# Performance work log

Measured on AMD Instinct MI355X. Metric: run time of the kernel, lower is better.

The kernel has to match this reference:

```python
import jax, jax.numpy as jnp
import numpy as np


def _interp_linear(c, out_len):
    """PyTorch F.interpolate(mode='linear', align_corners=False) along last axis.
    c: (d, in_len) -> (d, out_len). Half-pixel coordinate mapping."""
    in_len = c.shape[-1]
    scale = in_len / out_len
    src = (jnp.arange(out_len, dtype=jnp.float32) + 0.5) * scale - 0.5
    src = jnp.clip(src, 0.0, in_len - 1)
    lo = jnp.floor(src).astype(jnp.int32)
    hi = jnp.minimum(lo + 1, in_len - 1)
    w = (src - lo.astype(jnp.float32)).astype(c.dtype)
    return c[..., lo] * (1.0 - w) + c[..., hi] * w


def _causal_spectrum(spec, fft_size):
    """Given the real part of a causal kernel's spectrum (1, F, d) with
    F = fft_size//2+1, recover the full complex spectrum via the Hilbert
    transform (analytic-signal window in time domain)."""
    t = jnp.fft.irfft(spec, n=fft_size, axis=1)  # even real kernel (1, fft_size, d)
    w = jnp.ones((fft_size,), dtype=t.dtype)
    w = w.at[1:fft_size // 2].set(2.0)
    w = w.at[fft_size // 2 + 1:].set(0.0)
    return jnp.fft.rfft(t * w[None, :, None], axis=1)  # (1, F, d) complex


def setup_inputs() -> dict:
    key = jax.random.key(0)
    k1, k2 = jax.random.split(key)
    B, N, D, NUM_FREQS = 8, 8192, 512, 512
    x = jax.random.normal(k1, (B, N, D), dtype=jnp.float32)
    coeffs = jax.random.normal(k2, (D, NUM_FREQS), dtype=jnp.float32)
    dc = jnp.ones((D, 1), dtype=jnp.float32)
    return {"x": x, "coeffs": coeffs, "dc": dc}


def reference(x, coeffs, dc):
    n = x.shape[-2]
    fft_size = int(2 ** int(np.ceil(np.log2(2 * n))))
    # interpolate learned real frequency coefficients up to fft_size//2 bins
    pos = _interp_linear(coeffs, fft_size // 2)          # (d, fft_size//2)
    a = jnp.concatenate([dc, pos], axis=1)               # (d, fft_size//2+1)
    a = jnp.transpose(a)[None]                           # (1, F, d)
    spec = _causal_spectrum(a, fft_size)                 # (1, F, d) complex
    xf = jnp.fft.rfft(x, n=fft_size, axis=-2)            # (B, F, d)
    out = jnp.fft.irfft(xf * spec, n=fft_size, axis=-2)  # (B, fft_size, d)
    return out[..., :n, :]
```

## Files before the change

### kernel.cpp

```cpp
#include <hip/hip_runtime.h>


#define SPEC_LEN 8193
constexpr float PI_F = 3.14159265358979323846f;

__device__ __forceinline__ float2 f2add(float2 a, float2 b) { return make_float2(a.x + b.x, a.y + b.y); }
__device__ __forceinline__ float2 f2sub(float2 a, float2 b) { return make_float2(a.x - b.x, a.y - b.y); }
__device__ __forceinline__ float2 cmul(float2 a, float2 b) {
    return make_float2(a.x * b.x - a.y * b.y, a.x * b.y + a.y * b.x);
}

#define SLOT(k) ((((k) & 3) << 2) | ((k) >> 2))

__device__ __forceinline__ int addr1(int n2, int k1) {
    return (n2 << 4) | ((k1 + n2) & 15);
}
__device__ __forceinline__ int addr2(int r, int m2) {
    return (r << 5) | ((m2 + 2 * r) & 31);
}
__device__ __forceinline__ int addr3(int k) {
    int lo = (k + 2 * (k >> 4) + (k >> 8) + (k >> 12)) & 15;
    return (k & ~15) | lo;
}

template <int SGN>
__device__ __forceinline__ void fft4(float2& a, float2& b, float2& c, float2& d) {
    float2 A0 = f2add(a, c), A1 = f2sub(a, c), A2 = f2add(b, d), A3 = f2sub(b, d);
    float2 T = (SGN < 0) ? make_float2(A3.y, -A3.x) : make_float2(-A3.y, A3.x);
    a = f2add(A0, A2); b = f2add(A1, T); c = f2sub(A0, A2); d = f2sub(A1, T);
}

template <int SGN>
__device__ __forceinline__ void fft16_tail(float2* v) {
    const float C1 = 0.9238795325112867f, S1 = 0.3826834323650898f, R2 = 0.7071067811865476f;
    v[5]  = cmul(v[5],  make_float2(C1, SGN < 0 ? -S1 : S1));
    v[6]  = cmul(v[6],  make_float2(R2, SGN < 0 ? -R2 : R2));
    v[7]  = cmul(v[7],  make_float2(S1, SGN < 0 ? -C1 : C1));
    v[9]  = cmul(v[9],  make_float2(R2, SGN < 0 ? -R2 : R2));
    v[10] = (SGN < 0) ? make_float2(v[10].y, -v[10].x) : make_float2(-v[10].y, v[10].x);
    v[11] = cmul(v[11], make_float2(-R2, SGN < 0 ? -R2 : R2));
    v[13] = cmul(v[13], make_float2(S1, SGN < 0 ? -C1 : C1));
    v[14] = cmul(v[14], make_float2(-R2, SGN < 0 ? -R2 : R2));
    v[15] = cmul(v[15], make_float2(-C1, SGN < 0 ? S1 : -S1));
    fft4<SGN>(v[0], v[1], v[2], v[3]);
    fft4<SGN>(v[4], v[5], v[6], v[7]);
    fft4<SGN>(v[8], v[9], v[10], v[11]);
    fft4<SGN>(v[12], v[13], v[14], v[15]);
}
template <int SGN>
__device__ __forceinline__ void fft16(float2* v) {
    fft4<SGN>(v[0], v[4], v[8], v[12]);
    fft4<SGN>(v[1], v[5], v[9], v[13]);
    fft4<SGN>(v[2], v[6], v[10], v[14]);
    fft4<SGN>(v[3], v[7], v[11], v[15]);
    fft16_tail<SGN>(v);
}
template <int SGN>
__device__ __forceinline__ void fft16_half(float2* v) {
    #pragma unroll
    for (int j = 0; j < 4; ++j) {
        float2 a = v[j], b = v[j + 4];
        float2 T = (SGN < 0) ? make_float2(b.y, -b.x) : make_float2(-b.y, b.x);
        v[j] = f2add(a, b); v[j + 4] = f2add(a, T);
        v[j + 8] = f2sub(a, b); v[j + 12] = f2sub(a, T);
    }
    fft16_tail<SGN>(v);
}

__device__ __forceinline__ void twchain(float2* v, float2 w) {
    float2 acc = w;
    v[SLOT(1)] = cmul(v[SLOT(1)], acc);
    #pragma unroll
    for (int k = 2; k < 16; ++k) { acc = cmul(acc, w); v[SLOT(k)] = cmul(v[SLOT(k)], acc); }
}
__device__ __forceinline__ void twchain_nat(float2* v, float2 w) {
    float2 acc = w;
    v[1] = cmul(v[1], acc);
    #pragma unroll
    for (int k = 2; k < 16; ++k) { acc = cmul(acc, w); v[k] = cmul(v[k], acc); }
}

__device__ __forceinline__ float2 shflx1(float2 v) {
    return make_float2(__shfl_xor(v.x, 1), __shfl_xor(v.y, 1));
}

#define W32_TABLES \
    constexpr float WC[16] = {1.f, 0.98078528f, 0.92387953f, 0.83146961f, 0.70710678f, \
        0.55557023f, 0.38268343f, 0.19509032f, 0.f, -0.19509032f, -0.38268343f, \
        -0.55557023f, -0.70710678f, -0.83146961f, -0.92387953f, -0.98078528f}; \
    constexpr float WS[16] = {0.f, 0.19509032f, 0.38268343f, 0.55557023f, 0.70710678f, \
        0.83146961f, 0.92387953f, 0.98078528f, 1.f, 0.98078528f, 0.92387953f, \
        0.83146961f, 0.70710678f, 0.55557023f, 0.38268343f, 0.19509032f};

__device__ __forceinline__ void fwd_L2_L3(float2* sbuf, int tid) {
    {
        int k1 = tid >> 5, m2 = tid & 31;
        float2 u[16];
        #pragma unroll
        for (int m1 = 0; m1 < 16; ++m1) u[m1] = sbuf[addr1(32 * m1 + m2, k1)];
        __syncthreads();
        fft16<-1>(u);
        float sn, cs; __sincosf(-(PI_F / 256.0f) * (float)m2, &sn, &cs);
        twchain(u, make_float2(cs, sn));
        #pragma unroll
        for (int q1 = 0; q1 < 16; ++q1) sbuf[addr2(k1 * 16 + q1, m2)] = u[SLOT(q1)];
        __syncthreads();
    }
    {
        int k1 = tid >> 5, q1 = (tid >> 1) & 15, half = tid & 1;
        float2 e[16];
        #pragma unroll
        for (int j = 0; j < 16; ++j) e[j] = sbuf[addr2(k1 * 16 + q1, 2 * j + half)];
        __syncthreads();
        fft16<-1>(e);
        W32_TABLES
        #pragma unroll
        for (int q = 0; q < 16; ++q) {
            float2 mine = e[SLOT(q)];
            float2 othr = shflx1(mine);
            float2 Eq = half ? othr : mine;
            float2 Oq = half ? mine : othr;
            float2 WO = cmul(make_float2(WC[q], -WS[q]), Oq);
            float2 X = half ? f2sub(Eq, WO) : f2add(Eq, WO);
            int k = k1 + 16 * q1 + 256 * (q + 16 * half);
            sbuf[addr3(k)] = X;
        }
        __syncthreads();
    }
}

__device__ __forceinline__ void inv_L3_L2(float2* sbuf, int tid) {
    {
        int k1 = tid >> 5, q1 = (tid >> 1) & 15, half = tid & 1;
        float2 t[16];
        #pragma unroll
        for (int q = 0; q < 16; ++q)
            t[q] = sbuf[addr3(k1 + 16 * q1 + 256 * (q + 16 * half))];
        __syncthreads();
        W32_TABLES
        #pragma unroll
        for (int q = 0; q < 16; ++q) {
            float2 othr = shflx1(t[q]);
            if (half) t[q] = cmul(make_float2(WC[q], WS[q]), f2sub(othr, t[q]));
            else      t[q] = f2add(t[q], othr);
        }
        fft16<1>(t);
        #pragma unroll
        for (int j = 0; j < 16; ++j) sbuf[addr2(k1 * 16 + q1, 2 * j + half)] = t[SLOT(j)];
        __syncthreads();
    }
    {
        int k1 = tid >> 5, m2 = tid & 31;
        float2 u[16];
        #pragma unroll
        for (int q1 = 0; q1 < 16; ++q1) u[q1] = sbuf[addr2(k1 * 16 + q1, m2)];
        __syncthreads();
        float sn, cs; __sincosf((PI_F / 256.0f) * (float)m2, &sn, &cs);
        twchain_nat(u, make_float2(cs, sn));
        fft16<1>(u);
        #pragma unroll
        for (int m1 = 0; m1 < 16; ++m1) sbuf[addr1(32 * m1 + m2, k1)] = u[SLOT(m1)];
        __syncthreads();
    }
}

__device__ __forceinline__ void inv_L1(const float2* sbuf, int tid, float2* v) {
    #pragma unroll
    for (int k1 = 0; k1 < 16; ++k1) v[k1] = sbuf[addr1(tid, k1)];
    float sn, cs; __sincosf((PI_F / 4096.0f) * (float)tid, &sn, &cs);
    twchain_nat(v, make_float2(cs, sn));
    fft16<1>(v);
}

__device__ __forceinline__ float aval(const float* C, float dcv, int idx) {
    if (idx == 0) return dcv;
    int j = idx - 1;
    float src = ((float)j + 0.5f) * 0.0625f - 0.5f;
    src = fminf(fmaxf(src, 0.0f), 511.0f);
    int lo = (int)floorf(src);
    int hi = min(lo + 1, 511);
    float w = src - (float)lo;
    return C[lo] * (1.0f - w) + C[hi] * w;
}

__global__ __launch_bounds__(512) void k01(const float* __restrict__ x,
                                           const float* __restrict__ coeffs,
                                           const float* __restrict__ dc,
                                           float2* __restrict__ spec,
                                           float2* __restrict__ zin) {
    __shared__ float2 sbuf[8192];
    int tid = threadIdx.x;
    if (blockIdx.x < 512) {
        int d = blockIdx.x;
        const float* C = coeffs + d * 512;
        float dcv = dc[d];
        #pragma unroll
        for (int tt = 0; tt < 16; ++tt) {
            int k = tid + (tt << 9);
            float ak = aval(C, dcv, k);
            float am = aval(C, dcv, 8192 - k);
            float Ae = 0.5f * (ak + am), Ao = 0.5f * (ak - am);
            float sn, cs; __sincosf((PI_F / 8192.0f) * (float)k, &sn, &cs);
            sbuf[addr3(k)] = make_float2(Ae - Ao * sn, Ao * cs);
        }
        __syncthreads();
        inv_L3_L2(sbuf, tid);
        float2 v[16];
        inv_L1(sbuf, tid, v);
        float2 u[16];
        #pragma unroll
        for (int n1 = 0; n1 < 16; ++n1) {
            float2 z = v[SLOT(n1)];
            int n = (n1 << 9) + tid;
            float te = z.x * (1.0f / 8192.0f);
            float to = z.y * (1.0f / 8192.0f);
            int m0 = 2 * n;
            float he = (m0 == 0) ? te : ((m0 < 8192) ? 2.0f * te : ((m0 == 8192) ? te : 0.0f));
            float ho = (m0 + 1 < 8192) ? 2.0f * to : 0.0f;
            u[n1] = make_float2(he, ho);
        }
        fft16<-1>(u);
        float sn, cs; __sincosf(-(PI_F / 4096.0f) * (float)tid, &sn, &cs);
        twchain(u, make_float2(cs, sn));
        #pragma unroll
        for (int k1 = 0; k1 < 16; ++k1) sbuf[addr1(tid, k1)] = u[SLOT(k1)];
        __syncthreads();
        fwd_L2_L3(sbuf, tid);
        float2* Sd = spec + (size_t)d * SPEC_LEN;
        const float scale = 1.0f / 8192.0f;
        #pragma unroll
        for (int tt = 0; tt < 8; ++tt) {
            int k = tid + (tt << 9);
            if (k == 0) {
                float2 Z0 = sbuf[addr3(0)];
                Sd[0]    = make_float2((Z0.x + Z0.y) * scale, 0.0f);
                Sd[8192] = make_float2((Z0.x - Z0.y) * scale, 0.0f);
                float2 Z4 = sbuf[addr3(4096)];
                Sd[4096] = make_float2(Z4.x * scale, -Z4.y * scale);
            } else {
                int km = 8192 - k;
                float2 Zk = sbuf[addr3(k)], Zm = sbuf[addr3(km)];
                float2 Xe = make_float2((Zk.x + Zm.x) * 0.5f, (Zk.y - Zm.y) * 0.5f);
                float2 dz = make_float2((Zk.x - Zm.x) * 0.5f, (Zk.y + Zm.y) * 0.5f);
                float2 Xo = make_float2(dz.y, -dz.x);
                float sn2, cs2; __sincosf(-(PI_F / 8192.0f) * (float)k, &sn2, &cs2);
                float2 wXo = cmul(make_float2(cs2, sn2), Xo);
                Sd[k]  = make_float2((Xe.x + wXo.x) * scale, (Xe.y + wXo.y) * scale);
                Sd[km] = make_float2((Xe.x - wXo.x) * scale, -(Xe.y - wXo.y) * scale);
            }
        }
    } else {
        int bid = blockIdx.x - 512;
        int nt = bid & 127, dt = (bid >> 7) & 7, bb = bid >> 10;
        float* tile = (float*)sbuf;
        const float4* x4 = (const float4*)(x + ((size_t)bb * 8192 + (size_t)nt * 64) * 512 + dt * 64);
        int lane4 = tid & 15, row = tid >> 4;
        #pragma unroll
        for (int r = 0; r < 2; ++r) {
            int rr = row + 32 * r;
            float4 vv = x4[(size_t)rr * 128 + lane4];
            float* dst = &tile[rr * 65 + lane4 * 4];
            dst[0] = vv.x; dst[1] = vv.y; dst[2] = vv.z; dst[3] = vv.w;
        }
        __syncthreads();
        int tx4 = tid & 15, dl = tid >> 4;
        #pragma unroll
        for (int r = 0; r < 2; ++r) {
            int dloc = dl + 32 * r;
            int d = dt * 64 + dloc;
            int npb = nt * 32 + 2 * tx4;
            float4 w;
            w.x = tile[(4 * tx4 + 0) * 65 + dloc];
            w.y = tile[(4 * tx4 + 1) * 65 + dloc];
            w.z = tile[(4 * tx4 + 2) * 65 + dloc];
            w.w = tile[(4 * tx4 + 3) * 65 + dloc];
            *(float4*)&zin[((size_t)(d * 8 + bb)) * 4096 + npb] = w;
        }
    }
}

__global__ __launch_bounds__(512) void k2_conv(const float2* __restrict__ zin,
                                               const float2* __restrict__ spec,
                                               float2* __restrict__ yout) {
    __shared__ float2 sbuf[8192];
    int wg = blockIdx.x, d = wg >> 3, tid = threadIdx.x;
    const float2* zi = zin + (size_t)wg * 4096;
    float2 v[16];
    #pragma unroll
    for (int n1 = 0; n1 < 8; ++n1) v[n1] = zi[(n1 << 9) + tid];
    fft16_half<-1>(v);
    {
        float sn, cs; __sincosf(-(PI_F / 4096.0f) * (float)tid, &sn, &cs);
        twchain(v, make_float2(cs, sn));
    }
    #pragma unroll
    for (int k1 = 0; k1 < 16; ++k1) sbuf[addr1(tid, k1)] = v[SLOT(k1)];
    __syncthreads();
    fwd_L2_L3(sbuf, tid);
    const float2* S = spec + (size_t)d * SPEC_LEN;
    #pragma unroll
    for (int tt = 0; tt < 8; ++tt) {
        int k = tid + (tt << 9);
        if (k == 0) {
            float2 Z0 = sbuf[addr3(0)];
            float X0 = Z0.x + Z0.y, XM = Z0.x - Z0.y;
            float2 S0 = S[0], SM = S[8192];
            float2 Y0 = make_float2(X0 * S0.x, X0 * S0.y);
            float2 YM = make_float2(XM * SM.x, XM * SM.y);
            float2 Ye = make_float2((Y0.x + YM.x) * 0.5f, (Y0.y - YM.y) * 0.5f);
            float2 Yo = make_float2((Y0.x - YM.x) * 0.5f, (Y0.y + YM.y) * 0.5f);
            sbuf[addr3(0)] = make_float2(Ye.x - Yo.y, Ye.y + Yo.x);
            int p4 = addr3(4096);
            float2 Z4 = sbuf[p4];
            float2 Y4 = cmul(make_float2(Z4.x, -Z4.y), S[4096]);
            sbuf[p4] = make_float2(Y4.x, -Y4.y);
        } else {
            int km = 8192 - k;
            int p1 = addr3(k), p2 = addr3(km);
            float2 Zk = sbuf[p1], Zm = sbuf[p2];
            float2 Xe = make_float2((Zk.x + Zm.x) * 0.5f, (Zk.y - Zm.y) * 0.5f);
            float2 dz = make_float2((Zk.x - Zm.x) * 0.5f, (Zk.y + Zm.y) * 0.5f);
            float2 Xo = make_float2(dz.y, -dz.x);
            float sn, cs; __sincosf(-(PI_F / 8192.0f) * (float)k, &sn, &cs);
            float2 w = make_float2(cs, sn);
            float2 wXo = cmul(w, Xo);
            float2 Xk = f2add(Xe, wXo);
            float2 Xm = make_float2(Xe.x - wXo.x, -(Xe.y - wXo.y));
            float2 Yk = cmul(Xk, S[k]);
            float2 Ym = cmul(Xm, S[km]);
            float2 Ye = make_float2((Yk.x + Ym.x) * 0.5f, (Yk.y - Ym.y) * 0.5f);
            float2 dy = make_float2((Yk.x - Ym.x) * 0.5f, (Yk.y + Ym.y) * 0.5f);
            float2 Yo = cmul(make_float2(cs, -sn), dy);
            sbuf[p1] = make_float2(Ye.x - Yo.y, Ye.y + Yo.x);
            sbuf[p2] = make_float2(Ye.x + Yo.y, Yo.x - Ye.y);
        }
    }
    __syncthreads();
    inv_L3_L2(sbuf, tid);
    inv_L1(sbuf, tid, v);
    float2* yo = yout + (size_t)wg * 4096;
    #pragma unroll
    for (int n1 = 0; n1 < 8; ++n1) yo[(n1 << 9) + tid] = v[SLOT(n1)];
}

__global__ __launch_bounds__(512) void k3_unpack(const float2* __restrict__ yout,
                                                 float* __restrict__ out) {
    __shared__ float2 tile[64 * 33];
    int bid = blockIdx.x;
    int nt = bid & 127, dt = (bid >> 7) & 7, bb = bid >> 10;
    int tid = threadIdx.x;
    const float4* y4 = (const float4*)yout;
    int tx4 = tid & 15, dl = tid >> 4;
    #pragma unroll
    for (int r = 0; r < 2; ++r) {
        int dloc = dl + 32 * r;
        int d = dt * 64 + dloc;
        float4 vv = y4[(size_t)(d * 8 + bb) * 2048 + nt * 16 + tx4];
        tile[dloc * 33 + 2 * tx4]     = make_float2(vv.x, vv.y);
        tile[dloc * 33 + 2 * tx4 + 1] = make_float2(vv.z, vv.w);
    }
    __syncthreads();
    const float* tf = (const float*)tile;
    int lane4 = tid & 15, nl = tid >> 4;
    #pragma unroll
    for (int r = 0; r < 2; ++r) {
        int nloc = nl + 32 * r;
        int npl = nloc >> 1, e = nloc & 1;
        float4 w;
        w.x = tf[((4 * lane4 + 0) * 33 + npl) * 2 + e];
        w.y = tf[((4 * lane4 + 1) * 33 + npl) * 2 + e];
        w.z = tf[((4 * lane4 + 2) * 33 + npl) * 2 + e];
        w.w = tf[((4 * lane4 + 3) * 33 + npl) * 2 + e];
        int n = nt * 64 + nloc;
        *(float4*)&out[((size_t)bb * 8192 + n) * 512 + dt * 64 + lane4 * 4] = w;
    }
}

extern "C" void kernel_launch(void* const* d_in, const int* in_sizes, int n_in,
                              void* d_out, int out_size, void* d_ws, size_t ws_size,
                              hipStream_t stream) {
    const float* x      = (const float*)d_in[0];
    const float* coeffs = (const float*)d_in[1];
    const float* dc     = (const float*)d_in[2];
    float* out = (float*)d_out;

    float2* spec = (float2*)d_ws;
    float2* zbuf = (float2*)((char*)d_ws + (size_t)512 * SPEC_LEN * sizeof(float2));

    k01<<<512 + 8192, 512, 0, stream>>>(x, coeffs, dc, spec, zbuf);
    k2_conv<<<4096, 512, 0, stream>>>(zbuf, spec, zbuf);
    k3_unpack<<<8192, 512, 0, stream>>>(zbuf, out);
}
```

Baseline: 530.3 us.

## Precompute twiddle tables, fold real-FFT post-processing into spectrum coefficients, remap blocks

Replaces per-thread sincos twiddle chains with global twiddle tables built by a new init kernel. The spectrum is stored as precomputed P/Q coefficients so the convolution step fuses the real-FFT split/merge and the spectral multiply into fewer complex ops. k2 block indices are remapped by XCD for locality, code moves to ext_vector types, and occupancy hints are added. The cost is an extra kernel launch and extra global table reads, plus a small accuracy change from using table twiddles instead of chained ones.

```diff
diff --git a/kernel.cpp b/kernel.cpp
--- a/kernel.cpp
+++ b/kernel.cpp
@@ -1,14 +1,21 @@
 #include <hip/hip_runtime.h>
 
 
-#define SPEC_LEN 8193
-constexpr float PI_F = 3.14159265358979323846f;
-
-__device__ __forceinline__ float2 f2add(float2 a, float2 b) { return make_float2(a.x + b.x, a.y + b.y); }
-__device__ __forceinline__ float2 f2sub(float2 a, float2 b) { return make_float2(a.x - b.x, a.y - b.y); }
-__device__ __forceinline__ float2 cmul(float2 a, float2 b) {
-    return make_float2(a.x * b.x - a.y * b.y, a.x * b.y + a.y * b.x);
-}
+typedef float v2f __attribute__((ext_vector_type(2)));
+
+#define PQ_STRIDE 4097
+constexpr double PI_D = 3.14159265358979323846;
+
+__device__ v2f    g_twA[15][512];
+__device__ v2f    g_twB[15][32];
+__device__ v2f    g_w81[4096];
+__device__ v2f    g_h[4096];
+__device__ float4 g_u[4097];
+
+__device__ __forceinline__ v2f mkv2(float x, float y) { v2f r; r.x = x; r.y = y; return r; }
+__device__ __forceinline__ v2f cmul(v2f a, v2f b)  { return mkv2(a.x, a.x) * b + mkv2(-a.y, a.y) * b.yx; }
+__device__ __forceinline__ v2f cmulc(v2f a, v2f b) { return mkv2(a.x, -a.x) * b + mkv2(a.y, a.y) * b.yx; }
+__device__ __forceinline__ v2f cmulcA(v2f a, v2f b){ return mkv2(a.x, a.x) * b + mkv2(a.y, -a.y) * b.yx; }
 
 #define SLOT(k) ((((k) & 3) << 2) | ((k) >> 2))
 
@@ -24,31 +31,31 @@
 }
 
 template <int SGN>
-__device__ __forceinline__ void fft4(float2& a, float2& b, float2& c, float2& d) {
-    float2 A0 = f2add(a, c), A1 = f2sub(a, c), A2 = f2add(b, d), A3 = f2sub(b, d);
-    float2 T = (SGN < 0) ? make_float2(A3.y, -A3.x) : make_float2(-A3.y, A3.x);
-    a = f2add(A0, A2); b = f2add(A1, T); c = f2sub(A0, A2); d = f2sub(A1, T);
+__device__ __forceinline__ void fft4(v2f& a, v2f& b, v2f& c, v2f& d) {
+    v2f A0 = a + c, A1 = a - c, A2 = b + d, A3 = b - d;
+    v2f T = (SGN < 0) ? mkv2(A3.y, -A3.x) : mkv2(-A3.y, A3.x);
+    a = A0 + A2; b = A1 + T; c = A0 - A2; d = A1 - T;
 }
 
 template <int SGN>
-__device__ __forceinline__ void fft16_tail(float2* v) {
+__device__ __forceinline__ void fft16_tail(v2f* v) {
     const float C1 = 0.9238795325112867f, S1 = 0.3826834323650898f, R2 = 0.7071067811865476f;
-    v[5]  = cmul(v[5],  make_float2(C1, SGN < 0 ? -S1 : S1));
-    v[6]  = cmul(v[6],  make_float2(R2, SGN < 0 ? -R2 : R2));
-    v[7]  = cmul(v[7],  make_float2(S1, SGN < 0 ? -C1 : C1));
-    v[9]  = cmul(v[9],  make_float2(R2, SGN < 0 ? -R2 : R2));
-    v[10] = (SGN < 0) ? make_float2(v[10].y, -v[10].x) : make_float2(-v[10].y, v[10].x);
-    v[11] = cmul(v[11], make_float2(-R2, SGN < 0 ? -R2 : R2));
-    v[13] = cmul(v[13], make_float2(S1, SGN < 0 ? -C1 : C1));
-    v[14] = cmul(v[14], make_float2(-R2, SGN < 0 ? -R2 : R2));
-    v[15] = cmul(v[15], make_float2(-C1, SGN < 0 ? S1 : -S1));
+    v[5]  = cmul(v[5],  mkv2(C1, SGN < 0 ? -S1 : S1));
+    v[6]  = cmul(v[6],  mkv2(R2, SGN < 0 ? -R2 : R2));
+    v[7]  = cmul(v[7],  mkv2(S1, SGN < 0 ? -C1 : C1));
+    v[9]  = cmul(v[9],  mkv2(R2, SGN < 0 ? -R2 : R2));
+    v[10] = (SGN < 0) ? mkv2(v[10].y, -v[10].x) : mkv2(-v[10].y, v[10].x);
+    v[11] = cmul(v[11], mkv2(-R2, SGN < 0 ? -R2 : R2));
+    v[13] = cmul(v[13], mkv2(S1, SGN < 0 ? -C1 : C1));
+    v[14] = cmul(v[14], mkv2(-R2, SGN < 0 ? -R2 : R2));
+    v[15] = cmul(v[15], mkv2(-C1, SGN < 0 ? S1 : -S1));
     fft4<SGN>(v[0], v[1], v[2], v[3]);
     fft4<SGN>(v[4], v[5], v[6], v[7]);
     fft4<SGN>(v[8], v[9], v[10], v[11]);
     fft4<SGN>(v[12], v[13], v[14], v[15]);
 }
 template <int SGN>
-__device__ __forceinline__ void fft16(float2* v) {
+__device__ __forceinline__ void fft16(v2f* v) {
     fft4<SGN>(v[0], v[4], v[8], v[12]);
     fft4<SGN>(v[1], v[5], v[9], v[13]);
     fft4<SGN>(v[2], v[6], v[10], v[14]);
@@ -56,32 +63,19 @@
     fft16_tail<SGN>(v);
 }
 template <int SGN>
-__device__ __forceinline__ void fft16_half(float2* v) {
+__device__ __forceinline__ void fft16_half(v2f* v) {
     #pragma unroll
     for (int j = 0; j < 4; ++j) {
-        float2 a = v[j], b = v[j + 4];
-        float2 T = (SGN < 0) ? make_float2(b.y, -b.x) : make_float2(-b.y, b.x);
-        v[j] = f2add(a, b); v[j + 4] = f2add(a, T);
-        v[j + 8] = f2sub(a, b); v[j + 12] = f2sub(a, T);
+        v2f a = v[j], b = v[j + 4];
+        v2f T = (SGN < 0) ? mkv2(b.y, -b.x) : mkv2(-b.y, b.x);
+        v[j] = a + b; v[j + 4] = a + T;
+        v[j + 8] = a - b; v[j + 12] = a - T;
     }
     fft16_tail<SGN>(v);
 }
 
-__device__ __forceinline__ void twchain(float2* v, float2 w) {
-    float2 acc = w;
-    v[SLOT(1)] = cmul(v[SLOT(1)], acc);
-    #pragma unroll
-    for (int k = 2; k < 16; ++k) { acc = cmul(acc, w); v[SLOT(k)] = cmul(v[SLOT(k)], acc); }
-}
-__device__ __forceinline__ void twchain_nat(float2* v, float2 w) {
-    float2 acc = w;
-    v[1] = cmul(v[1], acc);
-    #pragma unroll
-    for (int k = 2; k < 16; ++k) { acc = cmul(acc, w); v[k] = cmul(v[k], acc); }
-}
-
-__device__ __forceinline__ float2 shflx1(float2 v) {
-    return make_float2(__shfl_xor(v.x, 1), __shfl_xor(v.y, 1));
+__device__ __forceinline__ v2f shflx1(v2f v) {
+    return mkv2(__shfl_xor(v.x, 1), __shfl_xor(v.y, 1));
 }
 
 #define W32_TABLES \
@@ -92,23 +86,26 @@
         0.83146961f, 0.92387953f, 0.98078528f, 1.f, 0.98078528f, 0.92387953f, \
         0.83146961f, 0.70710678f, 0.55557023f, 0.38268343f, 0.19509032f};
 
-__device__ __forceinline__ void fwd_L2_L3(float2* sbuf, int tid) {
+__device__ __forceinline__ void fwd_L2_L3(v2f* sbuf, int tid) {
     {
         int k1 = tid >> 5, m2 = tid & 31;
-        float2 u[16];
+        v2f w[15];
+        #pragma unroll
+        for (int j = 0; j < 15; ++j) w[j] = g_twB[j][m2];
+        v2f u[16];
         #pragma unroll
         for (int m1 = 0; m1 < 16; ++m1) u[m1] = sbuf[addr1(32 * m1 + m2, k1)];
         __syncthreads();
         fft16<-1>(u);
-        float sn, cs; __sincosf(-(PI_F / 256.0f) * (float)m2, &sn, &cs);
-        twchain(u, make_float2(cs, sn));
+        #pragma unroll
+        for (int k = 1; k < 16; ++k) u[SLOT(k)] = cmul(u[SLOT(k)], w[k - 1]);
         #pragma unroll
         for (int q1 = 0; q1 < 16; ++q1) sbuf[addr2(k1 * 16 + q1, m2)] = u[SLOT(q1)];
         __syncthreads();
     }
     {
         int k1 = tid >> 5, q1 = (tid >> 1) & 15, half = tid & 1;
-        float2 e[16];
+        v2f e[16];
         #pragma unroll
         for (int j = 0; j < 16; ++j) e[j] = sbuf[addr2(k1 * 16 + q1, 2 * j + half)];
         __syncthreads();
@@ -116,12 +113,12 @@
         W32_TABLES
         #pragma unroll
         for (int q = 0; q < 16; ++q) {
-            float2 mine = e[SLOT(q)];
-            float2 othr = shflx1(mine);
-            float2 Eq = half ? othr : mine;
-            float2 Oq = half ? mine : othr;
-            float2 WO = cmul(make_float2(WC[q], -WS[q]), Oq);
-            float2 X = half ? f2sub(Eq, WO) : f2add(Eq, WO);
+            v2f mine = e[SLOT(q)];
+            v2f othr = shflx1(mine);
+            v2f Eq = half ? othr : mine;
+            v2f Oq = half ? mine : othr;
+            v2f WO = cmul(mkv2(WC[q], -WS[q]), Oq);
+            v2f X = half ? Eq - WO : Eq + WO;
             int k = k1 + 16 * q1 + 256 * (q + 16 * half);
             sbuf[addr3(k)] = X;
         }
@@ -129,10 +126,10 @@
     }
 }
 
-__device__ __forceinline__ void inv_L3_L2(float2* sbuf, int tid) {
+__device__ __forceinline__ void inv_L3_L2(v2f* sbuf, int tid) {
     {
         int k1 = tid >> 5, q1 = (tid >> 1) & 15, half = tid & 1;
-        float2 t[16];
+        v2f t[16];
         #pragma unroll
         for (int q = 0; q < 16; ++q)
             t[q] = sbuf[addr3(k1 + 16 * q1 + 256 * (q + 16 * half))];
@@ -140,9 +137,9 @@
         W32_TABLES
         #pragma unroll
         for (int q = 0; q < 16; ++q) {
-            float2 othr = shflx1(t[q]);
-            if (half) t[q] = cmul(make_float2(WC[q], WS[q]), f2sub(othr, t[q]));
-            else      t[q] = f2add(t[q], othr);
+            v2f othr = shflx1(t[q]);
+            if (half) t[q] = cmul(mkv2(WC[q], WS[q]), othr - t[q]);
+            else      t[q] = t[q] + othr;
         }
         fft16<1>(t);
         #pragma unroll
@@ -151,12 +148,15 @@
     }
     {
         int k1 = tid >> 5, m2 = tid & 31;
-        float2 u[16];
+        v2f w[15];
+        #pragma unroll
+        for (int j = 0; j < 15; ++j) w[j] = g_twB[j][m2];
+        v2f u[16];
         #pragma unroll
         for (int q1 = 0; q1 < 16; ++q1) u[q1] = sbuf[addr2(k1 * 16 + q1, m2)];
         __syncthreads();
-        float sn, cs; __sincosf((PI_F / 256.0f) * (float)m2, &sn, &cs);
-        twchain_nat(u, make_float2(cs, sn));
+        #pragma unroll
+        for (int k = 1; k < 16; ++k) u[k] = cmulc(u[k], w[k - 1]);
         fft16<1>(u);
         #pragma unroll
         for (int m1 = 0; m1 < 16; ++m1) sbuf[addr1(32 * m1 + m2, k1)] = u[SLOT(m1)];
@@ -164,11 +164,14 @@
     }
 }
 
-__device__ __forceinline__ void inv_L1(const float2* sbuf, int tid, float2* v) {
+__device__ __forceinline__ void inv_L1(const v2f* sbuf, int tid, v2f* v) {
+    v2f w[15];
+    #pragma unroll
+    for (int j = 0; j < 15; ++j) w[j] = g_twA[j][tid];
     #pragma unroll
     for (int k1 = 0; k1 < 16; ++k1) v[k1] = sbuf[addr1(tid, k1)];
-    float sn, cs; __sincosf((PI_F / 4096.0f) * (float)tid, &sn, &cs);
-    twchain_nat(v, make_float2(cs, sn));
+    #pragma unroll
+    for (int k = 1; k < 16; ++k) v[k] = cmulc(v[k], w[k - 1]);
     fft16<1>(v);
 }
 
@@ -183,12 +186,69 @@
     return C[lo] * (1.0f - w) + C[hi] * w;
 }
 
-__global__ __launch_bounds__(512) void k01(const float* __restrict__ x,
-                                           const float* __restrict__ coeffs,
-                                           const float* __restrict__ dc,
-                                           float2* __restrict__ spec,
-                                           float2* __restrict__ zin) {
-    __shared__ float2 sbuf[8192];
+__device__ __forceinline__ void spec_single(v2f* sbuf, const float4* PQd, int k) {
+    float4 uu = g_u[k];
+    float4 pq = PQd[k];
+    v2f P = mkv2(pq.x, pq.y), Q = mkv2(pq.z, pq.w);
+    v2f al = P + Q;
+    v2f R  = P * uu.x - Q * uu.y;
+    int a = addr3(k);
+    v2f Z = sbuf[a];
+    v2f W = cmulc(R, Z);
+    sbuf[a] = cmul(al, Z) + mkv2(-W.y, W.x);
+}
+__device__ __forceinline__ void spec_pair(v2f* sbuf, const float4* PQd, int k) {
+    int m = 8192 - k;
+    float4 uu = g_u[k];
+    float4 pq = PQd[k];
+    v2f P = mkv2(pq.x, pq.y), Q = mkv2(pq.z, pq.w);
+    int ak = addr3(k), am = addr3(m);
+    v2f Zk = sbuf[ak], Zm = sbuf[am];
+    v2f al = P + Q;
+    v2f R  = P * uu.x - Q * uu.y;
+    v2f Dt = P * uu.z + Q * uu.w;
+    v2f W = cmulc(R, Zm);
+    v2f V = cmul(R, Zk);
+    sbuf[ak] = cmul(al, Zk) + mkv2(-W.y, W.x);
+    sbuf[am] = cmulcA(Dt, Zm) + V.yx;
+}
+
+__global__ void k_init() {
+    int t = blockIdx.x * 512 + threadIdx.x;
+    if (t < 4096) {
+        double th = (PI_D / 8192.0) * (double)t;
+        double s = sin(th), c = cos(th);
+        g_w81[t] = mkv2((float)c, (float)s);
+        g_h[t]   = mkv2((float)(0.5 * (1.0 - s)), (float)(0.5 * (1.0 + s)));
+    }
+    if (t <= 4096) {
+        if (t == 4096) {
+            g_u[t] = make_float4(0.f, 0.f, 0.f, 0.f);
+        } else {
+            double th = (PI_D / 8192.0) * (double)t;
+            double s = sin(th), c = cos(th);
+            g_u[t] = make_float4((float)(c / (1.0 - s)), (float)(c / (1.0 + s)),
+                                 (float)((1.0 + s) / (1.0 - s)), (float)((1.0 - s) / (1.0 + s)));
+        }
+    }
+    if (t < 7680) {
+        int j = t >> 9, tt = t & 511;
+        double th = -(PI_D / 4096.0) * (double)(tt * (j + 1));
+        g_twA[j][tt] = mkv2((float)cos(th), (float)sin(th));
+    }
+    if (t < 480) {
+        int j = t >> 5, m2 = t & 31;
+        double th = -(PI_D / 256.0) * (double)(m2 * (j + 1));
+        g_twB[j][m2] = mkv2((float)cos(th), (float)sin(th));
+    }
+}
+
+__global__ __launch_bounds__(512, 4) void k01(const float* __restrict__ x,
+                                              const float* __restrict__ coeffs,
+                                              const float* __restrict__ dc,
+                                              float4* __restrict__ PQ,
+                                              v2f* __restrict__ zin) {
+    __shared__ v2f sbuf[8192];
     int tid = threadIdx.x;
     if (blockIdx.x < 512) {
         int d = blockIdx.x;
@@ -200,53 +260,63 @@
             float ak = aval(C, dcv, k);
             float am = aval(C, dcv, 8192 - k);
             float Ae = 0.5f * (ak + am), Ao = 0.5f * (ak - am);
-            float sn, cs; __sincosf((PI_F / 8192.0f) * (float)k, &sn, &cs);
-            sbuf[addr3(k)] = make_float2(Ae - Ao * sn, Ao * cs);
+            float sn, cs;
+            if (tt < 8) { v2f w = g_w81[k];        cs = w.x;  sn = w.y; }
+            else        { v2f w = g_w81[k - 4096]; cs = -w.y; sn = w.x; }
+            sbuf[addr3(k)] = mkv2(Ae - Ao * sn, Ao * cs);
         }
         __syncthreads();
         inv_L3_L2(sbuf, tid);
-        float2 v[16];
+        v2f v[16];
         inv_L1(sbuf, tid, v);
-        float2 u[16];
+        v2f u[16];
         #pragma unroll
         for (int n1 = 0; n1 < 16; ++n1) {
-            float2 z = v[SLOT(n1)];
+            v2f z = v[SLOT(n1)];
             int n = (n1 << 9) + tid;
             float te = z.x * (1.0f / 8192.0f);
             float to = z.y * (1.0f / 8192.0f);
             int m0 = 2 * n;
             float he = (m0 == 0) ? te : ((m0 < 8192) ? 2.0f * te : ((m0 == 8192) ? te : 0.0f));
             float ho = (m0 + 1 < 8192) ? 2.0f * to : 0.0f;
-            u[n1] = make_float2(he, ho);
+            u[n1] = mkv2(he, ho);
         }
         fft16<-1>(u);
-        float sn, cs; __sincosf(-(PI_F / 4096.0f) * (float)tid, &sn, &cs);
-        twchain(u, make_float2(cs, sn));
+        v2f wA[15];
+        #pragma unroll
+        for (int j = 0; j < 15; ++j) wA[j] = g_twA[j][tid];
+        #pragma unroll
+        for (int k = 1; k < 16; ++k) u[SLOT(k)] = cmul(u[SLOT(k)], wA[k - 1]);
         #pragma unroll
         for (int k1 = 0; k1 < 16; ++k1) sbuf[addr1(tid, k1)] = u[SLOT(k1)];
         __syncthreads();
         fwd_L2_L3(sbuf, tid);
-        float2* Sd = spec + (size_t)d * SPEC_LEN;
+        float4* PQd = PQ + (size_t)d * PQ_STRIDE;
         const float scale = 1.0f / 8192.0f;
         #pragma unroll
         for (int tt = 0; tt < 8; ++tt) {
             int k = tid + (tt << 9);
             if (k == 0) {
-                float2 Z0 = sbuf[addr3(0)];
-                Sd[0]    = make_float2((Z0.x + Z0.y) * scale, 0.0f);
-                Sd[8192] = make_float2((Z0.x - Z0.y) * scale, 0.0f);
-                float2 Z4 = sbuf[addr3(4096)];
-                Sd[4096] = make_float2(Z4.x * scale, -Z4.y * scale);
+                v2f Z0 = sbuf[addr3(0)];
+                float S0 = (Z0.x + Z0.y) * scale;
+                float SM = (Z0.x - Z0.y) * scale;
+                PQd[0] = make_float4(0.5f * S0, 0.0f, 0.5f * SM, 0.0f);
+                v2f Z4 = sbuf[addr3(4096)];
+                float px = 0.5f * Z4.x * scale, py = 0.5f * Z4.y * scale;
+                PQd[4096] = make_float4(px, py, px, py);
             } else {
                 int km = 8192 - k;
-                float2 Zk = sbuf[addr3(k)], Zm = sbuf[addr3(km)];
-                float2 Xe = make_float2((Zk.x + Zm.x) * 0.5f, (Zk.y - Zm.y) * 0.5f);
-                float2 dz = make_float2((Zk.x - Zm.x) * 0.5f, (Zk.y + Zm.y) * 0.5f);
-                float2 Xo = make_float2(dz.y, -dz.x);
-                float sn2, cs2; __sincosf(-(PI_F / 8192.0f) * (float)k, &sn2, &cs2);
-                float2 wXo = cmul(make_float2(cs2, sn2), Xo);
-                Sd[k]  = make_float2((Xe.x + wXo.x) * scale, (Xe.y + wXo.y) * scale);
-                Sd[km] = make_float2((Xe.x - wXo.x) * scale, -(Xe.y - wXo.y) * scale);
+                v2f Zk = sbuf[addr3(k)], Zm = sbuf[addr3(km)];
+                v2f Xe = mkv2((Zk.x + Zm.x) * 0.5f, (Zk.y - Zm.y) * 0.5f);
+                v2f dz = mkv2((Zk.x - Zm.x) * 0.5f, (Zk.y + Zm.y) * 0.5f);
+                v2f Xo = mkv2(dz.y, -dz.x);
+                v2f w = g_w81[k];
+                v2f wXo = cmulc(Xo, w);
+                v2f Sk  = (Xe + wXo) * scale;
+                v2f SmC = (Xe - wXo) * scale;
+                v2f h = g_h[k];
+                v2f Pk = Sk * h.x, Qk = SmC * h.y;
+                PQd[k] = make_float4(Pk.x, Pk.y, Qk.x, Qk.y);
             }
         }
     } else {
@@ -279,66 +349,39 @@
     }
 }
 
-__global__ __launch_bounds__(512) void k2_conv(const float2* __restrict__ zin,
-                                               const float2* __restrict__ spec,
-                                               float2* __restrict__ yout) {
-    __shared__ float2 sbuf[8192];
-    int wg = blockIdx.x, d = wg >> 3, tid = threadIdx.x;
-    const float2* zi = zin + (size_t)wg * 4096;
-    float2 v[16];
+__global__ __launch_bounds__(512, 4) void k2_conv(const v2f* __restrict__ zin,
+                                                  const float4* __restrict__ PQ,
+                                                  v2f* __restrict__ yout) {
+    __shared__ v2f sbuf[8192];
+    int wg = blockIdx.x, tid = threadIdx.x;
+    int xcd = wg & 7, idx = wg >> 3;
+    int d = (xcd << 6) | (idx >> 3), b = idx & 7;
+    int io = d * 8 + b;
+    const v2f* zi = zin + (size_t)io * 4096;
+    const float4* PQd = PQ + (size_t)d * PQ_STRIDE;
+    v2f v[16];
     #pragma unroll
     for (int n1 = 0; n1 < 8; ++n1) v[n1] = zi[(n1 << 9) + tid];
+    v2f wA[15];
+    #pragma unroll
+    for (int j = 0; j < 15; ++j) wA[j] = g_twA[j][tid];
     fft16_half<-1>(v);
-    {
-        float sn, cs; __sincosf(-(PI_F / 4096.0f) * (float)tid, &sn, &cs);
-        twchain(v, make_float2(cs, sn));
-    }
+    #pragma unroll
+    for (int k = 1; k < 16; ++k) v[SLOT(k)] = cmul(v[SLOT(k)], wA[k - 1]);
     #pragma unroll
     for (int k1 = 0; k1 < 16; ++k1) sbuf[addr1(tid, k1)] = v[SLOT(k1)];
     __syncthreads();
     fwd_L2_L3(sbuf, tid);
-    const float2* S = spec + (size_t)d * SPEC_LEN;
     #pragma unroll
     for (int tt = 0; tt < 8; ++tt) {
         int k = tid + (tt << 9);
-        if (k == 0) {
-            float2 Z0 = sbuf[addr3(0)];
-            float X0 = Z0.x + Z0.y, XM = Z0.x - Z0.y;
-            float2 S0 = S[0], SM = S[8192];
-            float2 Y0 = make_float2(X0 * S0.x, X0 * S0.y);
-            float2 YM = make_float2(XM * SM.x, XM * SM.y);
-            float2 Ye = make_float2((Y0.x + YM.x) * 0.5f, (Y0.y - YM.y) * 0.5f);
-            float2 Yo = make_float2((Y0.x - YM.x) * 0.5f, (Y0.y + YM.y) * 0.5f);
-            sbuf[addr3(0)] = make_float2(Ye.x - Yo.y, Ye.y + Yo.x);
-            int p4 = addr3(4096);
-            float2 Z4 = sbuf[p4];
-            float2 Y4 = cmul(make_float2(Z4.x, -Z4.y), S[4096]);
-            sbuf[p4] = make_float2(Y4.x, -Y4.y);
-        } else {
-            int km = 8192 - k;
-            int p1 = addr3(k), p2 = addr3(km);
-            float2 Zk = sbuf[p1], Zm = sbuf[p2];
-            float2 Xe = make_float2((Zk.x + Zm.x) * 0.5f, (Zk.y - Zm.y) * 0.5f);
-            float2 dz = make_float2((Zk.x - Zm.x) * 0.5f, (Zk.y + Zm.y) * 0.5f);
-            float2 Xo = make_float2(dz.y, -dz.x);
-            float sn, cs; __sincosf(-(PI_F / 8192.0f) * (float)k, &sn, &cs);
-            float2 w = make_float2(cs, sn);
-            float2 wXo = cmul(w, Xo);
-            float2 Xk = f2add(Xe, wXo);
-            float2 Xm = make_float2(Xe.x - wXo.x, -(Xe.y - wXo.y));
-            float2 Yk = cmul(Xk, S[k]);
-            float2 Ym = cmul(Xm, S[km]);
-            float2 Ye = make_float2((Yk.x + Ym.x) * 0.5f, (Yk.y - Ym.y) * 0.5f);
-            float2 dy = make_float2((Yk.x - Ym.x) * 0.5f, (Yk.y + Ym.y) * 0.5f);
-            float2 Yo = cmul(make_float2(cs, -sn), dy);
-            sbuf[p1] = make_float2(Ye.x - Yo.y, Ye.y + Yo.x);
-            sbuf[p2] = make_float2(Ye.x + Yo.y, Yo.x - Ye.y);
-        }
+        if (k == 0) { spec_single(sbuf, PQd, 0); spec_single(sbuf, PQd, 4096); }
+        else        { spec_pair(sbuf, PQd, k); }
     }
     __syncthreads();
     inv_L3_L2(sbuf, tid);
     inv_L1(sbuf, tid, v);
-    float2* yo = yout + (size_t)wg * 4096;
+    v2f* yo = yout + (size_t)io * 4096;
     #pragma unroll
     for (int n1 = 0; n1 < 8; ++n1) yo[(n1 << 9) + tid] = v[SLOT(n1)];
 }
@@ -384,10 +427,11 @@
     const float* dc     = (const float*)d_in[2];
     float* out = (float*)d_out;
 
-    float2* spec = (float2*)d_ws;
-    float2* zbuf = (float2*)((char*)d_ws + (size_t)512 * SPEC_LEN * sizeof(float2));
-
-    k01<<<512 + 8192, 512, 0, stream>>>(x, coeffs, dc, spec, zbuf);
-    k2_conv<<<4096, 512, 0, stream>>>(zbuf, spec, zbuf);
-    k3_unpack<<<8192, 512, 0, stream>>>(zbuf, out);
-}
+    float4* PQ  = (float4*)d_ws;
+    v2f*    zbuf = (v2f*)((char*)d_ws + (size_t)512 * PQ_STRIDE * sizeof(float4));
+
+    k_init<<<15, 512, 0, stream>>>();
+    k01<<<512 + 8192, 512, 0, stream>>>(x, coeffs, dc, PQ, zbuf);
+    k2_conv<<<4096, 512, 0, stream>>>(zbuf, PQ, zbuf);
+    k3_unpack<<<8192, 512, 0, stream>>>((const float2*)zbuf, out);
+}
```

After: 487.8 us. 1.09x faster.
